# Kernel optimization log

Measured on AMD Instinct MI355X. Metric: run time of the kernel, lower is better.

Reference implementation:

```python
import jax, jax.numpy as jnp
import numpy as np

V, S, D, H = 32000, 1024, 768, 3072
EPS = 1e-5


def pos_encoding(seq_len, dim, dtype=jnp.float32):
    # pe[pos, i] = sin(pos/10000^(i/dim)) if i even else cos(pos/10000^(i/dim))
    pos = jnp.arange(seq_len, dtype=dtype)[:, None]
    i = jnp.arange(dim, dtype=dtype)[None, :]
    ang = pos / jnp.power(jnp.asarray(10000.0, dtype), i / dim)
    even = (jnp.arange(dim) % 2 == 0)[None, :]
    return jnp.where(even, jnp.sin(ang), jnp.cos(ang))


def layernorm2d(x, w, b):
    # normalizes over last two dims (token_size, input_dim), affine params [S, D]
    m = jnp.mean(x, axis=(-2, -1), keepdims=True)
    v = jnp.mean((x - m) ** 2, axis=(-2, -1), keepdims=True)
    return (x - m) / jnp.sqrt(v + EPS) * w + b


def setup_inputs() -> dict:
    key = jax.random.key(0)
    ks = jax.random.split(key, 16)
    sc = 0.02
    emb = jax.random.normal(ks[0], (V, D), jnp.float32) * sc
    emb = emb.at[0].set(0.0)  # padding_idx=0
    inp = {
        "x": jax.random.randint(ks[1], (8, S), 0, V),
        "emb": emb,
        "Wq": jax.random.normal(ks[2], (D, H), jnp.float32) * sc,
        "bq": jnp.zeros((H,), jnp.float32),
        "Wk": jax.random.normal(ks[3], (D, H), jnp.float32) * sc,
        "bk": jnp.zeros((H,), jnp.float32),
        "Wv": jax.random.normal(ks[4], (D, H), jnp.float32) * sc,
        "bv": jnp.zeros((H,), jnp.float32),
        "Wo": jax.random.normal(ks[5], (H, D), jnp.float32) * sc,
        "bo": jnp.zeros((D,), jnp.float32),
        "W1": jax.random.normal(ks[6], (D, H), jnp.float32) * sc,
        "b1": jnp.zeros((H,), jnp.float32),
        "W2": jax.random.normal(ks[7], (H, D), jnp.float32) * sc,
        "b2": jnp.zeros((D,), jnp.float32),
        "ln1_w": jnp.ones((S, D), jnp.float32),
        "ln1_b": jnp.zeros((S, D), jnp.float32),
        "ln2_w": jnp.ones((S, D), jnp.float32),
        "ln2_b": jnp.zeros((S, D), jnp.float32),
    }
    return inp


def reference(x, emb, Wq, bq, Wk, bk, Wv, bv, Wo, bo, W1, b1, W2, b2, ln1_w, ln1_b, ln2_w, ln2_b):
    y = emb[x]                                   # [B, S, D]
    y = y + pos_encoding(y.shape[1], y.shape[2], y.dtype)
    # unscaled self-attention (no 1/sqrt(d) factor, faithful to source)
    q = y @ Wq + bq
    k = y @ Wk + bk
    v = y @ Wv + bv
    attn = jax.nn.softmax(jnp.einsum("bsh,bth->bst", q, k), axis=-1)
    a = jnp.einsum("bst,bth->bsh", attn, v) @ Wo + bo
    y = layernorm2d(y + a, ln1_w, ln1_b)
    # FFN: GELU applied AFTER second linear (faithful to source)
    f = jax.nn.gelu((y @ W1 + b1) @ W2 + b2, approximate=False)
    y = layernorm2d(y + f, ln2_w, ln2_b)
    return y
```

## Files before the change

kernel.cpp:

```cpp
#include <hip/hip_runtime.h>
#include <hip/hip_fp16.h>

#define DI __device__ __forceinline__

typedef _Float16 f16x8 __attribute__((ext_vector_type(8)));
typedef float f32x4 __attribute__((ext_vector_type(4)));

struct alignas(8) h4 { __half x, y, z, w; };

DI void async16(const void* g, void* l) {
  __builtin_amdgcn_global_load_lds(
      (__attribute__((address_space(1))) void*)g,
      (__attribute__((address_space(3))) void*)l, 16, 0, 0);
}

DI float waveReduceSum(float v) {
#pragma unroll
  for (int i = 1; i < 64; i <<= 1) v += __shfl_xor(v, i);
  return v;
}
DI float waveReduceMax(float v) {
#pragma unroll
  for (int i = 1; i < 64; i <<= 1) v = fmaxf(v, __shfl_xor(v, i));
  return v;
}

DI float gelu_exact(float x) { return 0.5f * x * (1.f + erff(x * 0.70710678118654752f)); }

template <typename CT, bool BIAS, bool BROW>
__global__ __launch_bounds__(256) void gemm_nt(
    const __half* __restrict__ A, int lda, long long sA,
    const __half* __restrict__ Bt, int ldb, long long sB,
    const float* __restrict__ bias, long long sBias,
    CT* __restrict__ C, int ldc, long long sC,
    int nT, int K) {
  __shared__ __align__(16) __half As[128 * 64];
  __shared__ __align__(16) __half Bs[128 * 64];

  const int tid = threadIdx.x;
  const int wave = tid >> 6, lane = tid & 63;

  const int gsz = 8 * nT;
  const int g = blockIdx.x / gsz, r = blockIdx.x % gsz;
  const int m0 = (g * 8 + (r & 7)) * 128;
  const int n0 = (r >> 3) * 128;

  A += (long long)blockIdx.z * sA;
  Bt += (long long)blockIdx.z * sB;
  C += (long long)blockIdx.z * sC;
  if constexpr (BIAS || BROW) bias += (long long)blockIdx.z * sBias;
  const int wm = wave & 1, wn = wave >> 1;

  f32x4 acc[4][4];
#pragma unroll
  for (int i = 0; i < 4; ++i)
#pragma unroll
    for (int jj = 0; jj < 4; ++jj) acc[i][jj] = (f32x4){0.f, 0.f, 0.f, 0.f};

  const int srow = tid >> 3;
  const int gc = (tid & 7) ^ (srow & 7);
  const __half* Ag = A + (size_t)(m0 + srow) * lda + gc * 8;
  const __half* Bg = Bt + (size_t)(n0 + srow) * ldb + gc * 8;
  const size_t a32 = (size_t)32 * lda, b32 = (size_t)32 * ldb;
  char* AsW = (char*)As + wave * 1024;
  char* BsW = (char*)Bs + wave * 1024;

  const int ml = lane & 15, q = lane >> 4, lx = lane & 7;
  const int aoff = ((wm * 64 + ml) * 8 + (q ^ lx)) * 16;
  const int boff = ((wn * 64 + ml) * 8 + (q ^ lx)) * 16;

  for (int k0 = 0; k0 < K; k0 += 64) {
#pragma unroll
    for (int i = 0; i < 4; ++i) {
      async16(Ag + i * a32 + k0, AsW + i * 4096);
      async16(Bg + i * b32 + k0, BsW + i * 4096);
    }
    __syncthreads();
#pragma unroll
    for (int jj = 0; jj < 2; ++jj) {
      const char* Ab = (const char*)As + (jj ? (aoff ^ 64) : aoff);
      const char* Bb = (const char*)Bs + (jj ? (boff ^ 64) : boff);
      f16x8 af[4], bf[4];
#pragma unroll
      for (int i = 0; i < 4; ++i) {
        af[i] = *(const f16x8*)(Ab + i * 2048);
        bf[i] = *(const f16x8*)(Bb + i * 2048);
      }
#pragma unroll
      for (int i = 0; i < 4; ++i)
#pragma unroll
        for (int jn = 0; jn < 4; ++jn)
          acc[i][jn] = __builtin_amdgcn_mfma_f32_16x16x32_f16(af[i], bf[jn], acc[i][jn], 0, 0, 0);
    }
    __syncthreads();
  }

#pragma unroll
  for (int jj = 0; jj < 4; ++jj) {
    const int col = n0 + wn * 64 + jj * 16 + ml;
    const float bcol = BIAS ? bias[col] : 0.f;
#pragma unroll
    for (int i = 0; i < 4; ++i) {
      const int row = m0 + wm * 64 + i * 16 + q * 4;
#pragma unroll
      for (int rr = 0; rr < 4; ++rr) {
        float v = acc[i][jj][rr] + bcol;
        if constexpr (BROW) v += bias[row + rr];
        if constexpr (sizeof(CT) == 4)
          C[(size_t)(row + rr) * ldc + col] = v;
        else
          C[(size_t)(row + rr) * ldc + col] = __float2half(v);
      }
    }
  }
}

__global__ __launch_bounds__(256) void prep(
    const float* __restrict__ Wq, const float* __restrict__ Wk,
    const float* __restrict__ Wv, const float* __restrict__ W1,
    const float* __restrict__ Wo, const float* __restrict__ W2,
    const float* __restrict__ bq, const float* __restrict__ bk,
    __half* __restrict__ wD, __half* __restrict__ wB, __half* __restrict__ wC,
    __half* __restrict__ wA, float* __restrict__ bqk) {
  if (blockIdx.x == 2304) {
    if (blockIdx.y == 0)
      for (int i = threadIdx.x; i < 3072; i += 256) {
        bqk[i] = bq[i];
        bqk[3072 + i] = bk[i];
      }
    return;
  }
  __shared__ float t[32][33];
  const int tx = threadIdx.x & 31, ty = threadIdx.x >> 5;
  if (blockIdx.y < 4) {
    const float* in;
    __half* out;
    switch (blockIdx.y) {
      case 0: in = Wq; out = wD; break;
      case 1: in = Wk; out = wD + 3072 * 768; break;
      case 2: in = Wv; out = wB; break;
      default: in = W1; out = wC; break;
    }
    const int cb = blockIdx.x % 96, rb = blockIdx.x / 96;
    const int c = cb * 32 + tx, r0 = rb * 32;
#pragma unroll
    for (int i = 0; i < 32; i += 8) t[ty + i][tx] = in[(size_t)(r0 + ty + i) * 3072 + c];
    __syncthreads();
    const int oc = r0 + tx, o0 = cb * 32;
#pragma unroll
    for (int i = 0; i < 32; i += 8)
      out[(size_t)(o0 + ty + i) * 768 + oc] = __float2half(t[tx][ty + i]);
  } else {
    const float* in = (blockIdx.y == 5) ? W2 : Wo;
    __half* out = wA + ((blockIdx.y == 5) ? 3072 * 768 : 0);
    const int cb = blockIdx.x % 24, rb = blockIdx.x / 24;
    const int c = cb * 32 + tx, r0 = rb * 32;
#pragma unroll
    for (int i = 0; i < 32; i += 8) t[ty + i][tx] = in[(size_t)(r0 + ty + i) * 768 + c];
    __syncthreads();
    const int oc = r0 + tx, o0 = cb * 32;
#pragma unroll
    for (int i = 0; i < 32; i += 8)
      out[(size_t)(o0 + ty + i) * 3072 + oc] = __float2half(t[tx][ty + i]);
  }
}

__global__ __launch_bounds__(256) void embed_pos_kernel(
    const int* __restrict__ x, const float* __restrict__ emb,
    float* __restrict__ y, __half* __restrict__ yh) {
  const int row = blockIdx.x;
  const int s = row & 1023;
  const int tok = x[row];
  const float* ep = emb + (size_t)tok * 768;
  float* yp = y + (size_t)row * 768;
  __half* hp = yh + (size_t)row * 768;
  const float c = -13.287712379549449f / 768.f;
  for (int d = threadIdx.x; d < 768; d += 256) {
    float ang = (float)s * exp2f((float)d * c);
    float pe = (d & 1) ? cosf(ang) : sinf(ang);
    float v = ep[d] + pe;
    yp[d] = v;
    hp[d] = __float2half(v);
  }
}

__global__ __launch_bounds__(256) void softmax_rows(
    const float* __restrict__ L, __half* __restrict__ P) {
  const size_t row = blockIdx.x;
  const float4 x = ((const float4*)(L + row * 1024))[threadIdx.x];
  const int wave = threadIdx.x >> 6, lane = threadIdx.x & 63;
  float m = fmaxf(fmaxf(x.x, x.y), fmaxf(x.z, x.w));
  m = waveReduceMax(m);
  __shared__ float sm[4];
  __shared__ float ssum[4];
  if (lane == 0) sm[wave] = m;
  __syncthreads();
  m = fmaxf(fmaxf(sm[0], sm[1]), fmaxf(sm[2], sm[3]));
  float e0 = expf(x.x - m), e1 = expf(x.y - m), e2 = expf(x.z - m), e3 = expf(x.w - m);
  float s = e0 + e1 + e2 + e3;
  s = waveReduceSum(s);
  if (lane == 0) ssum[wave] = s;
  __syncthreads();
  s = ssum[0] + ssum[1] + ssum[2] + ssum[3];
  const float inv = 1.f / s;
  h4 o{__float2half(e0 * inv), __float2half(e1 * inv), __float2half(e2 * inv),
       __float2half(e3 * inv)};
  ((h4*)(P + row * 1024))[threadIdx.x] = o;
}

template <bool GELU>
__global__ __launch_bounds__(256) void residual_stats(
    float* __restrict__ y, const float* __restrict__ p0, const float* __restrict__ p1,
    const float* __restrict__ bias, float2* __restrict__ partials) {
  const int b = blockIdx.y, chunk = blockIdx.x;
  const size_t base = (size_t)b * 786432 + (size_t)chunk * 8192;
  float4* yp = (float4*)(y + base);
  const float4* a0 = (const float4*)(p0 + base);
  const float4* a1 = (const float4*)(p1 + base);
  float s = 0.f, ss = 0.f;
#pragma unroll
  for (int it = 0; it < 8; ++it) {
    const int idx = it * 256 + threadIdx.x;
    const int d = (chunk * 8192 + it * 1024 + threadIdx.x * 4) % 768;
    float4 yv = yp[idx];
    float4 v0 = a0[idx];
    float4 v1 = a1[idx];
    const float4 bv = *(const float4*)(bias + d);
    float ax = v0.x + v1.x + bv.x, ay = v0.y + v1.y + bv.y;
    float az = v0.z + v1.z + bv.z, aw = v0.w + v1.w + bv.w;
    if constexpr (GELU) {
      ax = gelu_exact(ax); ay = gelu_exact(ay);
      az = gelu_exact(az); aw = gelu_exact(aw);
    }
    float4 r{yv.x + ax, yv.y + ay, yv.z + az, yv.w + aw};
    yp[idx] = r;
    s += r.x + r.y + r.z + r.w;
    ss += r.x * r.x + r.y * r.y + r.z * r.z + r.w * r.w;
  }
  s = waveReduceSum(s);
  ss = waveReduceSum(ss);
  __shared__ float2 wr[4];
  const int wave = threadIdx.x >> 6, lane = threadIdx.x & 63;
  if (lane == 0) wr[wave] = make_float2(s, ss);
  __syncthreads();
  if (threadIdx.x == 0) {
    float S = wr[0].x + wr[1].x + wr[2].x + wr[3].x;
    float SS = wr[0].y + wr[1].y + wr[2].y + wr[3].y;
    partials[b * 96 + chunk] = make_float2(S, SS);
  }
}

template <bool WB>
__global__ __launch_bounds__(256) void ln_apply(
    float* __restrict__ y, __half* __restrict__ yh, const float* __restrict__ w,
    const float* __restrict__ bb, const float2* __restrict__ partials) {
  const unsigned i4 = blockIdx.x * 256 + threadIdx.x;
  const unsigned i = i4 * 4;
  const unsigned b = i / 786432u;
  const int tid = threadIdx.x;
  float s = 0.f, ss = 0.f;
  if (tid < 96) {
    float2 p = partials[b * 96 + tid];
    s = p.x;
    ss = p.y;
  }
  s = waveReduceSum(s);
  ss = waveReduceSum(ss);
  __shared__ float2 wsum[4];
  if ((tid & 63) == 0) wsum[tid >> 6] = make_float2(s, ss);
  __syncthreads();
  const float S = wsum[0].x + wsum[1].x + wsum[2].x + wsum[3].x;
  const float SS = wsum[0].y + wsum[1].y + wsum[2].y + wsum[3].y;
  const float inv = 1.f / 786432.f;
  const float mean = S * inv;
  const float rstd = rsqrtf(SS * inv - mean * mean + 1e-5f);

  const unsigned e4 = (i - b * 786432u) >> 2;
  float4 yv = ((const float4*)y)[i4];
  const float4 wv = ((const float4*)w)[e4];
  const float4 bv = ((const float4*)bb)[e4];
  float4 r;
  r.x = (yv.x - mean) * rstd * wv.x + bv.x;
  r.y = (yv.y - mean) * rstd * wv.y + bv.y;
  r.z = (yv.z - mean) * rstd * wv.z + bv.z;
  r.w = (yv.w - mean) * rstd * wv.w + bv.w;
  ((float4*)y)[i4] = r;
  if constexpr (WB) {
    h4 o{__float2half(r.x), __float2half(r.y), __float2half(r.z), __float2half(r.w)};
    ((h4*)yh)[i4] = o;
  }
}

extern "C" void kernel_launch(void* const* d_in, const int* in_sizes, int n_in,
                              void* d_out, int out_size, void* d_ws, size_t ws_size,
                              hipStream_t stream) {
  const int* x = (const int*)d_in[0];
  const float* emb = (const float*)d_in[1];
  const float* Wq = (const float*)d_in[2];
  const float* bq = (const float*)d_in[3];
  const float* Wk = (const float*)d_in[4];
  const float* bk = (const float*)d_in[5];
  const float* Wv = (const float*)d_in[6];
  const float* bv = (const float*)d_in[7];
  const float* Wo = (const float*)d_in[8];
  const float* bo = (const float*)d_in[9];
  const float* W1 = (const float*)d_in[10];
  const float* b1 = (const float*)d_in[11];
  const float* W2 = (const float*)d_in[12];
  const float* b2 = (const float*)d_in[13];
  const float* ln1w = (const float*)d_in[14];
  const float* ln1b = (const float*)d_in[15];
  const float* ln2w = (const float*)d_in[16];
  const float* ln2b = (const float*)d_in[17];

  float* y = (float*)d_out;

  char* ws = (char*)d_ws;
  __half* yh = (__half*)(ws + 0);
  __half* qb = (__half*)(ws + 12582912);
  __half* kb = (__half*)(ws + 62914560);
  __half* Ph = kb;
  __half* vT = (__half*)(ws + 113246208);
  float* abuf = (float*)vT;
  float* Lg = (float*)(ws + 163577856);
  __half* wA = (__half*)(ws + 197132288);
  __half* wD = (__half*)(ws + 206569472);
  __half* wB = (__half*)(ws + 216006656);
  __half* wC = (__half*)(ws + 220725248);
  float* bqk = (float*)(ws + 225443840);
  float2* part = (float2*)(ws + 225468416);
  const size_t WS_NEEDED = 225474624;
  if (ws_size < WS_NEEDED) return;

  const dim3 blk(256);
  const long long SH = 1024LL * 3072, SS = 1024LL * 1024;
  const long long HALF = 25165824;
  float* p1 = abuf + 6291456;

  prep<<<dim3(2305, 6), blk, 0, stream>>>(Wq, Wk, Wv, W1, Wo, W2, bq, bk, wD, wB, wC, wA, bqk);
  embed_pos_kernel<<<dim3(8192), blk, 0, stream>>>(x, emb, y, yh);

  gemm_nt<__half, true, false><<<dim3(1536, 1, 2), blk, 0, stream>>>(
      yh, 768, 0, wD, 768, 3072LL * 768, bqk, 3072, qb, 3072, HALF, 24, 768);

  gemm_nt<__half, false, true><<<dim3(192, 1, 8), blk, 0, stream>>>(
      wB, 768, 0, yh, 768, 1024LL * 768, bv, 0, vT, 1024, SH, 8, 768);

  gemm_nt<float, false, false><<<dim3(64, 1, 8), blk, 0, stream>>>(
      qb, 3072, SH, kb, 3072, SH, nullptr, 0, Lg, 1024, SS, 8, 3072);

  softmax_rows<<<dim3(8192), blk, 0, stream>>>(Lg, Ph);

  gemm_nt<__half, false, false><<<dim3(192, 1, 8), blk, 0, stream>>>(
      Ph, 1024, SS, vT, 1024, SH, nullptr, 0, (__half*)qb, 3072, SH, 24, 1024);

  gemm_nt<float, false, false><<<dim3(384, 1, 2), blk, 0, stream>>>(
      (__half*)qb, 3072, 1536, wA, 3072, 1536, nullptr, 0, abuf, 768, 6291456, 6, 1536);

  residual_stats<false><<<dim3(96, 8), blk, 0, stream>>>(y, abuf, p1, bo, part);
  ln_apply<true><<<dim3(6144), blk, 0, stream>>>(y, yh, ln1w, ln1b, part);

  gemm_nt<__half, true, false><<<dim3(1536, 1, 1), blk, 0, stream>>>(
      yh, 768, 0, wC, 768, 0, b1, 0, (__half*)qb, 3072, 0, 24, 768);
  gemm_nt<float, false, false><<<dim3(384, 1, 2), blk, 0, stream>>>(
      (__half*)qb, 3072, 1536, wA + 3072 * 768, 3072, 1536, nullptr, 0, abuf, 768, 6291456, 6, 1536);

  residual_stats<true><<<dim3(96, 8), blk, 0, stream>>>(y, abuf, p1, b2, part);
  ln_apply<false><<<dim3(6144), blk, 0, stream>>>(y, nullptr, ln2w, ln2b, part);
}
```

Measured before the change: 739.6 us.

## Add 256x256-tile 8-wave double-buffered GEMM and use it for most matmuls

```diff
diff --git a/kernel.cpp b/kernel.cpp
--- a/kernel.cpp
+++ b/kernel.cpp
@@ -26,6 +26,172 @@
 }
 
 DI float gelu_exact(float x) { return 0.5f * x * (1.f + erff(x * 0.70710678118654752f)); }
+
+template <typename CT, bool BIAS, bool BROW>
+__global__ __launch_bounds__(512, 2) void gemm_nt8(
+    const __half* __restrict__ A, int lda, long long sA,
+    const __half* __restrict__ Bt, int ldb, long long sB,
+    const float* __restrict__ bias, long long sBias,
+    CT* __restrict__ C, int ldc, long long sC,
+    int nT, int K) {
+  __shared__ __align__(16) __half As[2][16384];
+  __shared__ __align__(16) __half Bs[2][16384];
+
+  const int tid = threadIdx.x;
+  const int wave = tid >> 6, lane = tid & 63;
+
+  const int gsz = 4 * nT;
+  const int g = blockIdx.x / gsz, r = blockIdx.x % gsz;
+  const int m0 = (g * 4 + (r & 3)) * 256;
+  const int n0 = (r >> 2) * 256;
+
+  A += (long long)blockIdx.z * sA;
+  Bt += (long long)blockIdx.z * sB;
+  C += (long long)blockIdx.z * sC;
+  if constexpr (BIAS || BROW) bias += (long long)blockIdx.z * sBias;
+
+  const int wm = wave >> 2, wn = wave & 3;
+
+  f32x4 acc[8][4];
+#pragma unroll
+  for (int i = 0; i < 8; ++i)
+#pragma unroll
+    for (int j = 0; j < 4; ++j) acc[i][j] = (f32x4){0.f, 0.f, 0.f, 0.f};
+
+  const int srow = tid >> 3;
+  const int gc = (tid & 7) ^ (srow & 7);
+  const __half* Ag = A + (size_t)(m0 + srow) * lda + gc * 8;
+  const __half* Bg = Bt + (size_t)(n0 + srow) * ldb + gc * 8;
+  const size_t a64 = (size_t)64 * lda, b64 = (size_t)64 * ldb;
+  char* AsW = (char*)As + wave * 1024;
+  char* BsW = (char*)Bs + wave * 1024;
+
+#define STG_A(t)                                                      \
+  {                                                                   \
+    const __half* s_ = Ag + (t) * 64;                                 \
+    char* d_ = AsW + (((t) & 1) ? 32768 : 0);                         \
+    async16(s_, d_);                                                  \
+    async16(s_ + a64, d_ + 8192);                                     \
+    async16(s_ + 2 * a64, d_ + 16384);                                \
+    async16(s_ + 3 * a64, d_ + 24576);                                \
+  }
+#define STG_B(t)                                                      \
+  {                                                                   \
+    const __half* s_ = Bg + (t) * 64;                                 \
+    char* d_ = BsW + (((t) & 1) ? 32768 : 0);                         \
+    async16(s_, d_);                                                  \
+    async16(s_ + b64, d_ + 8192);                                     \
+    async16(s_ + 2 * b64, d_ + 16384);                                \
+    async16(s_ + 3 * b64, d_ + 24576);                                \
+  }
+
+  const int ml = lane & 15, q = lane >> 4, lx = lane & 7;
+  const int co0 = (q ^ lx) * 16, co1 = co0 ^ 64;
+  const char* Ar = (const char*)As + wm * 16384 + ml * 128;
+  const char* Br = (const char*)Bs + (wn >> 1) * 16384 + (wn & 1) * 8192 + ml * 128;
+
+  const int nt = K >> 6;
+  STG_A(0);
+  STG_B(0);
+  if (nt > 1) {
+    STG_A(1);
+    STG_B(1);
+    asm volatile("s_waitcnt vmcnt(8)" ::: "memory");
+  } else {
+    asm volatile("s_waitcnt vmcnt(0)" ::: "memory");
+  }
+  __builtin_amdgcn_s_barrier();
+
+  for (int t = 0; t < nt; ++t) {
+    const int pb = (t & 1) ? 32768 : 0;
+    const char* Ap = Ar + pb;
+    const char* Bp = Br + pb;
+    f16x8 a0[4], a1[4], a2[4], a3[4], b0[4], b1[4];
+
+#pragma unroll
+    for (int i = 0; i < 4; ++i) a0[i] = *(const f16x8*)(Ap + i * 2048 + co0);
+#pragma unroll
+    for (int j = 0; j < 4; ++j) b0[j] = *(const f16x8*)(Bp + j * 2048 + co0);
+    __builtin_amdgcn_s_barrier();
+    asm volatile("s_waitcnt lgkmcnt(0)" ::: "memory");
+    __builtin_amdgcn_s_setprio(1);
+#pragma unroll
+    for (int i = 0; i < 4; ++i)
+#pragma unroll
+      for (int j = 0; j < 4; ++j)
+        acc[i][j] = __builtin_amdgcn_mfma_f32_16x16x32_f16(a0[i], b0[j], acc[i][j], 0, 0, 0);
+    __builtin_amdgcn_s_setprio(0);
+    __builtin_amdgcn_s_barrier();
+
+#pragma unroll
+    for (int i = 0; i < 4; ++i) a1[i] = *(const f16x8*)(Ap + (4 + i) * 2048 + co0);
+#pragma unroll
+    for (int j = 0; j < 4; ++j) b1[j] = *(const f16x8*)(Bp + j * 2048 + co1);
+    __builtin_amdgcn_s_barrier();
+    asm volatile("s_waitcnt lgkmcnt(0)" ::: "memory");
+    __builtin_amdgcn_s_setprio(1);
+#pragma unroll
+    for (int i = 0; i < 4; ++i)
+#pragma unroll
+      for (int j = 0; j < 4; ++j)
+        acc[4 + i][j] = __builtin_amdgcn_mfma_f32_16x16x32_f16(a1[i], b0[j], acc[4 + i][j], 0, 0, 0);
+    __builtin_amdgcn_s_setprio(0);
+    __builtin_amdgcn_s_barrier();
+
+#pragma unroll
+    for (int i = 0; i < 4; ++i) a2[i] = *(const f16x8*)(Ap + i * 2048 + co1);
+#pragma unroll
+    for (int i = 0; i < 4; ++i) a3[i] = *(const f16x8*)(Ap + (4 + i) * 2048 + co1);
+    if (t + 2 < nt) STG_B(t + 2);
+    __builtin_amdgcn_s_barrier();
+    asm volatile("s_waitcnt lgkmcnt(0)" ::: "memory");
+    __builtin_amdgcn_s_setprio(1);
+#pragma unroll
+    for (int i = 0; i < 4; ++i)
+#pragma unroll
+      for (int j = 0; j < 4; ++j)
+        acc[i][j] = __builtin_amdgcn_mfma_f32_16x16x32_f16(a2[i], b1[j], acc[i][j], 0, 0, 0);
+    __builtin_amdgcn_s_setprio(0);
+    __builtin_amdgcn_s_barrier();
+
+    if (t + 2 < nt) {
+      STG_A(t + 2);
+      asm volatile("s_waitcnt vmcnt(8)" ::: "memory");
+    } else if (t + 1 < nt) {
+      asm volatile("s_waitcnt vmcnt(0)" ::: "memory");
+    }
+    __builtin_amdgcn_s_barrier();
+    __builtin_amdgcn_s_setprio(1);
+#pragma unroll
+    for (int i = 0; i < 4; ++i)
+#pragma unroll
+      for (int j = 0; j < 4; ++j)
+        acc[4 + i][j] = __builtin_amdgcn_mfma_f32_16x16x32_f16(a3[i], b1[j], acc[4 + i][j], 0, 0, 0);
+    __builtin_amdgcn_s_setprio(0);
+    __builtin_amdgcn_s_barrier();
+  }
+#undef STG_A
+#undef STG_B
+
+#pragma unroll
+  for (int j = 0; j < 4; ++j) {
+    const int col = n0 + wn * 64 + j * 16 + ml;
+    const float bcol = BIAS ? bias[col] : 0.f;
+#pragma unroll
+    for (int i = 0; i < 8; ++i) {
+      const int row = m0 + wm * 128 + i * 16 + q * 4;
+#pragma unroll
+      for (int rr = 0; rr < 4; ++rr) {
+        float v = acc[i][j][rr] + bcol;
+        if constexpr (BROW) v += bias[row + rr];
+        if constexpr (sizeof(CT) == 4)
+          C[(size_t)(row + rr) * ldc + col] = v;
+        else
+          C[(size_t)(row + rr) * ldc + col] = __float2half(v);
+      }
+    }
+  }
+}
 
 template <typename CT, bool BIAS, bool BROW>
 __global__ __launch_bounds__(256) void gemm_nt(
@@ -332,7 +498,7 @@
   const size_t WS_NEEDED = 225474624;
   if (ws_size < WS_NEEDED) return;
 
-  const dim3 blk(256);
+  const dim3 blk(256), blk8(512);
   const long long SH = 1024LL * 3072, SS = 1024LL * 1024;
   const long long HALF = 25165824;
   float* p1 = abuf + 6291456;
@@ -340,30 +506,30 @@
   prep<<<dim3(2305, 6), blk, 0, stream>>>(Wq, Wk, Wv, W1, Wo, W2, bq, bk, wD, wB, wC, wA, bqk);
   embed_pos_kernel<<<dim3(8192), blk, 0, stream>>>(x, emb, y, yh);
 
-  gemm_nt<__half, true, false><<<dim3(1536, 1, 2), blk, 0, stream>>>(
-      yh, 768, 0, wD, 768, 3072LL * 768, bqk, 3072, qb, 3072, HALF, 24, 768);
-
-  gemm_nt<__half, false, true><<<dim3(192, 1, 8), blk, 0, stream>>>(
-      wB, 768, 0, yh, 768, 1024LL * 768, bv, 0, vT, 1024, SH, 8, 768);
+  gemm_nt8<__half, true, false><<<dim3(384, 1, 2), blk8, 0, stream>>>(
+      yh, 768, 0, wD, 768, 3072LL * 768, bqk, 3072, qb, 3072, HALF, 12, 768);
+
+  gemm_nt8<__half, false, true><<<dim3(48, 1, 8), blk8, 0, stream>>>(
+      wB, 768, 0, yh, 768, 1024LL * 768, bv, 0, vT, 1024, SH, 4, 768);
 
   gemm_nt<float, false, false><<<dim3(64, 1, 8), blk, 0, stream>>>(
       qb, 3072, SH, kb, 3072, SH, nullptr, 0, Lg, 1024, SS, 8, 3072);
 
   softmax_rows<<<dim3(8192), blk, 0, stream>>>(Lg, Ph);
 
-  gemm_nt<__half, false, false><<<dim3(192, 1, 8), blk, 0, stream>>>(
-      Ph, 1024, SS, vT, 1024, SH, nullptr, 0, (__half*)qb, 3072, SH, 24, 1024);
-
-  gemm_nt<float, false, false><<<dim3(384, 1, 2), blk, 0, stream>>>(
-      (__half*)qb, 3072, 1536, wA, 3072, 1536, nullptr, 0, abuf, 768, 6291456, 6, 1536);
+  gemm_nt8<__half, false, false><<<dim3(48, 1, 8), blk8, 0, stream>>>(
+      Ph, 1024, SS, vT, 1024, SH, nullptr, 0, (__half*)qb, 3072, SH, 12, 1024);
+
+  gemm_nt8<float, false, false><<<dim3(96, 1, 2), blk8, 0, stream>>>(
+      (__half*)qb, 3072, 1536, wA, 3072, 1536, nullptr, 0, abuf, 768, 6291456, 3, 1536);
 
   residual_stats<false><<<dim3(96, 8), blk, 0, stream>>>(y, abuf, p1, bo, part);
   ln_apply<true><<<dim3(6144), blk, 0, stream>>>(y, yh, ln1w, ln1b, part);
 
-  gemm_nt<__half, true, false><<<dim3(1536, 1, 1), blk, 0, stream>>>(
-      yh, 768, 0, wC, 768, 0, b1, 0, (__half*)qb, 3072, 0, 24, 768);
-  gemm_nt<float, false, false><<<dim3(384, 1, 2), blk, 0, stream>>>(
-      (__half*)qb, 3072, 1536, wA + 3072 * 768, 3072, 1536, nullptr, 0, abuf, 768, 6291456, 6, 1536);
+  gemm_nt8<__half, true, false><<<dim3(384, 1, 1), blk8, 0, stream>>>(
+      yh, 768, 0, wC, 768, 0, b1, 0, (__half*)qb, 3072, 0, 12, 768);
+  gemm_nt8<float, false, false><<<dim3(96, 1, 2), blk8, 0, stream>>>(
+      (__half*)qb, 3072, 1536, wA + 3072 * 768, 3072, 1536, nullptr, 0, abuf, 768, 6291456, 3, 1536);
 
   residual_stats<true><<<dim3(96, 8), blk, 0, stream>>>(y, abuf, p1, b2, part);
   ln_apply<false><<<dim3(6144), blk, 0, stream>>>(y, nullptr, ln2w, ln2b, part);
```

Measured after the change: 836.2 us. 13.1% more time.

## Add 256x256 double-buffered 8-wave GEMM for Q/K projection; vectorize epilogue stores

Applied to the files above, without the earlier changes.

```diff
diff --git a/kernel.cpp b/kernel.cpp
--- a/kernel.cpp
+++ b/kernel.cpp
@@ -26,6 +26,139 @@
 }
 
 DI float gelu_exact(float x) { return 0.5f * x * (1.f + erff(x * 0.70710678118654752f)); }
+
+template <typename CT, bool BIAS, bool BROW>
+__global__ __launch_bounds__(512, 2) void gemm_nt8(
+    const __half* __restrict__ A, int lda, long long sA,
+    const __half* __restrict__ Bt, int ldb, long long sB,
+    const float* __restrict__ bias, long long sBias,
+    CT* __restrict__ C, int ldc, long long sC,
+    int nT, int K) {
+  __shared__ __align__(16) __half As[2][16384];
+  __shared__ __align__(16) __half Bs[2][16384];
+
+  const int tid = threadIdx.x;
+  const int wave = tid >> 6, lane = tid & 63;
+
+  const int gsz = 4 * nT;
+  const int g = blockIdx.x / gsz, r = blockIdx.x % gsz;
+  const int m0 = (g * 4 + (r & 3)) * 256;
+  const int n0 = (r >> 2) * 256;
+
+  A += (long long)blockIdx.z * sA;
+  Bt += (long long)blockIdx.z * sB;
+  C += (long long)blockIdx.z * sC;
+  if constexpr (BIAS || BROW) bias += (long long)blockIdx.z * sBias;
+
+  const int wm = wave >> 2, wn = wave & 3;
+
+  f32x4 acc[8][4];
+#pragma unroll
+  for (int i = 0; i < 8; ++i)
+#pragma unroll
+    for (int j = 0; j < 4; ++j) acc[i][j] = (f32x4){0.f, 0.f, 0.f, 0.f};
+
+  const int srow = tid >> 3;
+  const int gc = (tid & 7) ^ (srow & 7);
+  const __half* Ag = A + (size_t)(m0 + srow) * lda + gc * 8;
+  const __half* Bg = Bt + (size_t)(n0 + srow) * ldb + gc * 8;
+  const size_t a64 = (size_t)64 * lda, b64 = (size_t)64 * ldb;
+  char* AsWr = (char*)As + wave * 1024 + lane * 16;
+  char* BsWr = (char*)Bs + wave * 1024 + lane * 16;
+
+  f16x8 sra[4], srb[4];
+
+#define LDG(t)                                                        \
+  {                                                                   \
+    const __half* sa_ = Ag + (t) * 64;                                \
+    const __half* sb_ = Bg + (t) * 64;                                \
+    sra[0] = *(const f16x8*)(sa_);                                    \
+    sra[1] = *(const f16x8*)(sa_ + a64);                              \
+    sra[2] = *(const f16x8*)(sa_ + 2 * a64);                          \
+    sra[3] = *(const f16x8*)(sa_ + 3 * a64);                          \
+    srb[0] = *(const f16x8*)(sb_);                                    \
+    srb[1] = *(const f16x8*)(sb_ + b64);                              \
+    srb[2] = *(const f16x8*)(sb_ + 2 * b64);                          \
+    srb[3] = *(const f16x8*)(sb_ + 3 * b64);                          \
+  }
+#define DSW(t)                                                        \
+  {                                                                   \
+    char* da_ = AsWr + (((t) & 1) ? 32768 : 0);                       \
+    char* db_ = BsWr + (((t) & 1) ? 32768 : 0);                       \
+    *(f16x8*)(da_) = sra[0];                                          \
+    *(f16x8*)(da_ + 8192) = sra[1];                                   \
+    *(f16x8*)(da_ + 16384) = sra[2];                                  \
+    *(f16x8*)(da_ + 24576) = sra[3];                                  \
+    *(f16x8*)(db_) = srb[0];                                          \
+    *(f16x8*)(db_ + 8192) = srb[1];                                   \
+    *(f16x8*)(db_ + 16384) = srb[2];                                  \
+    *(f16x8*)(db_ + 24576) = srb[3];                                  \
+  }
+
+  const int ml = lane & 15, q = lane >> 4, lx = lane & 7;
+  const int co0 = (q ^ lx) * 16, co1 = co0 ^ 64;
+  const char* Ar = (const char*)As + wm * 16384 + ml * 128;
+  const char* Br = (const char*)Bs + (wn >> 1) * 16384 + (wn & 1) * 8192 + ml * 128;
+
+  const int nt = K >> 6;
+  LDG(0);
+  DSW(0);
+  if (nt > 1) LDG(1);
+  asm volatile("s_waitcnt lgkmcnt(0)" ::: "memory");
+  __builtin_amdgcn_s_barrier();
+  __builtin_amdgcn_sched_barrier(0);
+
+  for (int t = 0; t < nt; ++t) {
+    if (t + 1 < nt) {
+      DSW(t + 1);
+      if (t + 2 < nt) LDG(t + 2);
+    }
+    const int pb = (t & 1) ? 32768 : 0;
+    const char* Ap = Ar + pb;
+    const char* Bp = Br + pb;
+    f16x8 af[8], bf[4];
+#pragma unroll
+    for (int ks = 0; ks < 2; ++ks) {
+      const int co = ks ? co1 : co0;
+#pragma unroll
+      for (int i = 0; i < 8; ++i) af[i] = *(const f16x8*)(Ap + i * 2048 + co);
+#pragma unroll
+      for (int j = 0; j < 4; ++j) bf[j] = *(const f16x8*)(Bp + j * 2048 + co);
+#pragma unroll
+      for (int i = 0; i < 8; ++i)
+#pragma unroll
+        for (int j = 0; j < 4; ++j)
+          acc[i][j] = __builtin_amdgcn_mfma_f32_16x16x32_f16(bf[j], af[i], acc[i][j], 0, 0, 0);
+    }
+    asm volatile("s_waitcnt lgkmcnt(0)" ::: "memory");
+    __builtin_amdgcn_s_barrier();
+    __builtin_amdgcn_sched_barrier(0);
+  }
+#undef LDG
+#undef DSW
+
+#pragma unroll
+  for (int j = 0; j < 4; ++j) {
+    const int col0 = n0 + wn * 64 + j * 16 + q * 4;
+    float4 bc = {0.f, 0.f, 0.f, 0.f};
+    if constexpr (BIAS) bc = *(const float4*)(bias + col0);
+#pragma unroll
+    for (int i = 0; i < 8; ++i) {
+      const int row = m0 + wm * 128 + i * 16 + ml;
+      const float br = BROW ? bias[row] : 0.f;
+      const float v0 = acc[i][j][0] + bc.x + br;
+      const float v1 = acc[i][j][1] + bc.y + br;
+      const float v2 = acc[i][j][2] + bc.z + br;
+      const float v3 = acc[i][j][3] + bc.w + br;
+      if constexpr (sizeof(CT) == 4) {
+        *(float4*)(C + (size_t)row * ldc + col0) = make_float4(v0, v1, v2, v3);
+      } else {
+        h4 o{__float2half(v0), __float2half(v1), __float2half(v2), __float2half(v3)};
+        *(h4*)((__half*)C + (size_t)row * ldc + col0) = o;
+      }
+    }
+  }
+}
 
 template <typename CT, bool BIAS, bool BROW>
 __global__ __launch_bounds__(256) void gemm_nt(
@@ -90,26 +223,29 @@
       for (int i = 0; i < 4; ++i)
 #pragma unroll
         for (int jn = 0; jn < 4; ++jn)
-          acc[i][jn] = __builtin_amdgcn_mfma_f32_16x16x32_f16(af[i], bf[jn], acc[i][jn], 0, 0, 0);
+          acc[i][jn] = __builtin_amdgcn_mfma_f32_16x16x32_f16(bf[jn], af[i], acc[i][jn], 0, 0, 0);
     }
     __syncthreads();
   }
 
 #pragma unroll
-  for (int jj = 0; jj < 4; ++jj) {
-    const int col = n0 + wn * 64 + jj * 16 + ml;
-    const float bcol = BIAS ? bias[col] : 0.f;
+  for (int jn = 0; jn < 4; ++jn) {
+    const int col0 = n0 + wn * 64 + jn * 16 + q * 4;
+    float4 bc = {0.f, 0.f, 0.f, 0.f};
+    if constexpr (BIAS) bc = *(const float4*)(bias + col0);
 #pragma unroll
     for (int i = 0; i < 4; ++i) {
-      const int row = m0 + wm * 64 + i * 16 + q * 4;
-#pragma unroll
-      for (int rr = 0; rr < 4; ++rr) {
-        float v = acc[i][jj][rr] + bcol;
-        if constexpr (BROW) v += bias[row + rr];
-        if constexpr (sizeof(CT) == 4)
-          C[(size_t)(row + rr) * ldc + col] = v;
-        else
-          C[(size_t)(row + rr) * ldc + col] = __float2half(v);
+      const int row = m0 + wm * 64 + i * 16 + ml;
+      const float br = BROW ? bias[row] : 0.f;
+      const float v0 = acc[i][jn][0] + bc.x + br;
+      const float v1 = acc[i][jn][1] + bc.y + br;
+      const float v2 = acc[i][jn][2] + bc.z + br;
+      const float v3 = acc[i][jn][3] + bc.w + br;
+      if constexpr (sizeof(CT) == 4) {
+        *(float4*)(C + (size_t)row * ldc + col0) = make_float4(v0, v1, v2, v3);
+      } else {
+        h4 o{__float2half(v0), __float2half(v1), __float2half(v2), __float2half(v3)};
+        *(h4*)((__half*)C + (size_t)row * ldc + col0) = o;
       }
     }
   }
@@ -332,7 +468,7 @@
   const size_t WS_NEEDED = 225474624;
   if (ws_size < WS_NEEDED) return;
 
-  const dim3 blk(256);
+  const dim3 blk(256), blk8(512);
   const long long SH = 1024LL * 3072, SS = 1024LL * 1024;
   const long long HALF = 25165824;
   float* p1 = abuf + 6291456;
@@ -340,8 +476,8 @@
   prep<<<dim3(2305, 6), blk, 0, stream>>>(Wq, Wk, Wv, W1, Wo, W2, bq, bk, wD, wB, wC, wA, bqk);
   embed_pos_kernel<<<dim3(8192), blk, 0, stream>>>(x, emb, y, yh);
 
-  gemm_nt<__half, true, false><<<dim3(1536, 1, 2), blk, 0, stream>>>(
-      yh, 768, 0, wD, 768, 3072LL * 768, bqk, 3072, qb, 3072, HALF, 24, 768);
+  gemm_nt8<__half, true, false><<<dim3(384, 1, 2), blk8, 0, stream>>>(
+      yh, 768, 0, wD, 768, 3072LL * 768, bqk, 3072, qb, 3072, HALF, 12, 768);
 
   gemm_nt<__half, false, true><<<dim3(192, 1, 8), blk, 0, stream>>>(
       wB, 768, 0, yh, 768, 1024LL * 768, bv, 0, vT, 1024, SH, 8, 768);
```

Result: no change. 743.4 us (+0.5%).
